# Optimization experiments

Hardware: AMD Instinct MI355X
Metric: run time of the kernel (lower is better)

Reference implementation:

```python
import jax, jax.numpy as jnp
import numpy as np

P, N, D = 8, 1024, 768
H = 12
HS = D // H
SCALE = float(HS ** 0.5)  # NOTE: original multiplies by sqrt(head_size)


def setup_inputs() -> dict:
    key = jax.random.key(0)
    k1, k2, k3 = jax.random.split(key, 3)
    pixel_values = jax.random.normal(k1, (P, N, D), dtype=jnp.float32)
    attention_mask = jnp.zeros((P, 1, 1, N), dtype=jnp.float32)
    qkv_w = jax.random.normal(k2, (D, 3 * D), dtype=jnp.float32) * 0.02
    qkv_b = jnp.zeros((3 * D,), dtype=jnp.float32)
    proj_w = jax.random.normal(k3, (D, D), dtype=jnp.float32) * 0.02
    proj_b = jnp.zeros((D,), dtype=jnp.float32)
    return {
        "pixel_values": pixel_values,
        "attention_mask": attention_mask,
        "qkv_w": qkv_w,
        "qkv_b": qkv_b,
        "proj_w": proj_w,
        "proj_b": proj_b,
    }


def reference(pixel_values, attention_mask, qkv_w, qkv_b, proj_w, proj_b):
    p, n, d = pixel_values.shape
    # fused QKV projection: (p, n, 3d) -> (3, p, H, n, hs)
    mixed = pixel_values @ qkv_w + qkv_b
    mixed = mixed.reshape(p, n, 3, H, HS).transpose(2, 0, 3, 1, 4)
    q, k, v = mixed[0], mixed[1], mixed[2]
    # scores: (p, H, n, n); original multiplies by sqrt(head_size)
    scores = jnp.einsum("phqd,phkd->phqk", q, k) * SCALE
    probs = jax.nn.softmax(scores, axis=-1)
    # dropout p=0 (identity in eval); mask added POST-softmax, per source
    probs = probs + attention_mask
    ctx = jnp.einsum("phqk,phkd->phqd", probs, v)
    ctx = ctx.transpose(0, 2, 1, 3).reshape(p, n, d)
    out = ctx @ proj_w + proj_b
    return out
```

## Files before the change

kernel.cpp:

```cpp
#include <hip/hip_runtime.h>
#include <hip/hip_bf16.h>
#include <cstdint>
#include <math.h>

constexpr int PB = 8;
constexpr int NS = 1024;
constexpr int DM = 768;
constexpr int NH = 12;
constexpr int HSZ = 64;
constexpr float EOFF = 88.0f;

typedef short bf16x8 __attribute__((ext_vector_type(8)));
typedef _Float16 half8 __attribute__((ext_vector_type(8)));
typedef float floatx4 __attribute__((ext_vector_type(4)));

__device__ __forceinline__ ushort f2bf(float x) {
    __hip_bfloat16 b = __float2bfloat16(x);
    return *reinterpret_cast<ushort*>(&b);
}
__device__ __forceinline__ float bf2f(ushort u) {
    __hip_bfloat16 b = *reinterpret_cast<__hip_bfloat16*>(&u);
    return __bfloat162float(b);
}
__device__ __forceinline__ ushort f2h(float x) {
    _Float16 h = (_Float16)x;
    return *reinterpret_cast<ushort*>(&h);
}

#define GLDS(g, l)                                                             \
    __builtin_amdgcn_global_load_lds(                                          \
        (const __attribute__((address_space(1))) void*)(g),                    \
        (__attribute__((address_space(3))) void*)(l), 16, 0, 0)

__global__ void split_kernel(const float* __restrict__ x, ushort* __restrict__ bh,
                             ushort* __restrict__ hf, int n4)
{
    int i = blockIdx.x * blockDim.x + threadIdx.x;
    const int stride = gridDim.x * blockDim.x;
    for (; i < n4; i += stride) {
        const float4 v = ((const float4*)x)[i];
        ((ushort4*)bh)[i] = ushort4{f2bf(v.x), f2bf(v.y), f2bf(v.z), f2bf(v.w)};
        ((ushort4*)hf)[i] = ushort4{f2h(v.x),  f2h(v.y),  f2h(v.z),  f2h(v.w)};
    }
}

__global__ void splitT_kernel(const float* __restrict__ w, ushort* __restrict__ bT,
                              ushort* __restrict__ fT, int K, int N)
{
    __shared__ float tile[32][33];
    const int tx = threadIdx.x, ty = threadIdx.y;
    const int bx = blockIdx.x, by = blockIdx.y;
    #pragma unroll
    for (int r = 0; r < 4; ++r)
        tile[ty + r*8][tx] = w[(size_t)(by*32 + ty + r*8) * N + bx*32 + tx];
    __syncthreads();
    #pragma unroll
    for (int r = 0; r < 4; ++r) {
        const int n = bx*32 + ty + r*8;
        const int k = by*32 + tx;
        const float v = tile[tx][ty + r*8];
        bT[(size_t)n * K + k] = f2bf(v);
        if (fT) fT[(size_t)n * K + k] = f2h(v);
    }
}

__global__ __launch_bounds__(256, 3)
void gemm_qkf(const ushort* __restrict__ Af, const ushort* __restrict__ Bf,
              const float* __restrict__ bias,
              ushort* __restrict__ qf, ushort* __restrict__ kf, int K)
{
    __shared__ __align__(16) ushort As[128*64];
    __shared__ __align__(16) ushort Bs[128*64];

    const int t    = threadIdx.x;
    const int w    = t >> 6;
    const int lane = t & 63;
    const int l15  = lane & 15;
    const int quad = lane >> 4;
    const int wm = w >> 1, wn = w & 1;
    const int m0 = blockIdx.x * 128, n0 = blockIdx.y * 128;

    floatx4 acc[4][4];
    #pragma unroll
    for (int i = 0; i < 4; ++i)
        #pragma unroll
        for (int j = 0; j < 4; ++j) acc[i][j] = floatx4{0.f, 0.f, 0.f, 0.f};

    const int srow8 = lane >> 3;
    const int sslot = lane & 7;

    for (int k0 = 0; k0 < K; k0 += 64) {
        #pragma unroll
        for (int j = 0; j < 4; ++j) {
            const int row = w*32 + j*8 + srow8;
            const int seg = sslot ^ (row & 7);
            const int ldst = (w*32 + j*8) * 64;
            GLDS(Af + (size_t)(m0 + row) * K + k0 + seg*8, As + ldst);
            GLDS(Bf + (size_t)(n0 + row) * K + k0 + seg*8, Bs + ldst);
        }
        __syncthreads();

        #pragma unroll
        for (int h2 = 0; h2 < 2; ++h2) {
            half8 fa[4], fb[4];
            #pragma unroll
            for (int i = 0; i < 4; ++i) {
                const int sl = ((h2*4 + quad) ^ (l15 & 7)) * 8;
                fa[i] = *(const half8*)(As + (wm*64 + i*16 + l15) * 64 + sl);
                fb[i] = *(const half8*)(Bs + (wn*64 + i*16 + l15) * 64 + sl);
            }
            #pragma unroll
            for (int mt = 0; mt < 4; ++mt)
                #pragma unroll
                for (int nt = 0; nt < 4; ++nt)
                    acc[mt][nt] = __builtin_amdgcn_mfma_f32_16x16x32_f16(fa[mt], fb[nt], acc[mt][nt], 0, 0, 0);
        }
        __syncthreads();
    }

    const int jbase = n0 + wn*64;
    const int c  = jbase / DM;
    const int hh = (jbase % DM) >> 6;
    const int pp = (m0 + wm*64) >> 10;
    const size_t head = (size_t)pp * NH + hh;
    ushort* dst = (c == 0 ? qf : kf);
    const float qscale = (c == 0) ? 8.0f : 1.0f;
    #pragma unroll
    for (int nt = 0; nt < 4; ++nt) {
        const int s = nt*16 + l15;
        const float bval = bias[jbase + s];
        #pragma unroll
        for (int mt = 0; mt < 4; ++mt) {
            const int tok0 = m0 + wm*64 + mt*16 + quad*4;
            const int nn0  = tok0 & 1023;
            #pragma unroll
            for (int r = 0; r < 4; ++r)
                dst[(head*NS + nn0 + r) * HSZ + s] = f2h((acc[mt][nt][r] + bval) * qscale);
        }
    }
}

template <int MODE>
__global__ __launch_bounds__(256, 3)
void gemm_1p(const ushort* __restrict__ Ah, const ushort* __restrict__ Bh,
             const float* __restrict__ bias, float* __restrict__ outf,
             ushort* __restrict__ vt, int K)
{
    __shared__ __align__(16) ushort As[128*64];
    __shared__ __align__(16) ushort Bs[128*64];

    const int t    = threadIdx.x;
    const int w    = t >> 6;
    const int lane = t & 63;
    const int l15  = lane & 15;
    const int quad = lane >> 4;
    const int wm = w >> 1, wn = w & 1;
    const int m0 = blockIdx.x * 128, n0 = blockIdx.y * 128;

    floatx4 acc[4][4];
    #pragma unroll
    for (int i = 0; i < 4; ++i)
        #pragma unroll
        for (int j = 0; j < 4; ++j) acc[i][j] = floatx4{0.f, 0.f, 0.f, 0.f};

    const int srow8 = lane >> 3;
    const int sslot = lane & 7;

    for (int k0 = 0; k0 < K; k0 += 64) {
        #pragma unroll
        for (int j = 0; j < 4; ++j) {
            const int row = w*32 + j*8 + srow8;
            const int seg = sslot ^ (row & 7);
            const int ldst = (w*32 + j*8) * 64;
            GLDS(Ah + (size_t)(m0 + row) * K + k0 + seg*8, As + ldst);
            GLDS(Bh + (size_t)(n0 + row) * K + k0 + seg*8, Bs + ldst);
        }
        __syncthreads();

        #pragma unroll
        for (int h2 = 0; h2 < 2; ++h2) {
            bf16x8 fa[4], fb[4];
            #pragma unroll
            for (int i = 0; i < 4; ++i) {
                const int sl = ((h2*4 + quad) ^ (l15 & 7)) * 8;
                fa[i] = *(const bf16x8*)(As + (wm*64 + i*16 + l15) * 64 + sl);
                fb[i] = *(const bf16x8*)(Bs + (wn*64 + i*16 + l15) * 64 + sl);
            }
            #pragma unroll
            for (int mt = 0; mt < 4; ++mt)
                #pragma unroll
                for (int nt = 0; nt < 4; ++nt)
                    acc[mt][nt] = __builtin_amdgcn_mfma_f32_16x16x32_bf16(fa[mt], fb[nt], acc[mt][nt], 0, 0, 0);
        }
        __syncthreads();
    }

    if (MODE == 0) {
        #pragma unroll
        for (int nt = 0; nt < 4; ++nt) {
            const int col = n0 + wn*64 + nt*16 + l15;
            const float bval = bias[col];
            #pragma unroll
            for (int mt = 0; mt < 4; ++mt) {
                const int row0 = m0 + wm*64 + mt*16 + quad*4;
                #pragma unroll
                for (int r = 0; r < 4; ++r)
                    outf[(size_t)(row0 + r) * DM + col] = acc[mt][nt][r] + bval;
            }
        }
    } else {
        const int jbase = n0 + wn*64;
        const int hh = jbase >> 6;
        const int pp = (m0 + wm*64) >> 10;
        const size_t head = (size_t)pp * NH + hh;
        #pragma unroll
        for (int nt = 0; nt < 4; ++nt) {
            const int s = nt*16 + l15;
            const float bval = bias[jbase + s];
            #pragma unroll
            for (int mt = 0; mt < 4; ++mt) {
                const int tok0 = m0 + wm*64 + mt*16 + quad*4;
                const int nn0  = tok0 & 1023;
                ushort4 pk;
                pk.x = f2bf(acc[mt][nt][0] + bval);
                pk.y = f2bf(acc[mt][nt][1] + bval);
                pk.z = f2bf(acc[mt][nt][2] + bval);
                pk.w = f2bf(acc[mt][nt][3] + bval);
                *(ushort4*)(vt + (head*HSZ + s) * NS + nn0) = pk;
            }
        }
    }
}

__global__ void mv_kernel(const float* __restrict__ mask, const ushort* __restrict__ vt,
                          float* __restrict__ mv)
{
    __shared__ float red[4][64];
    const int ph = blockIdx.x;
    const int t  = threadIdx.x;
    const int c  = t & 63, part = t >> 6;
    const ushort* vrow = vt + ((size_t)ph * HSZ + c) * NS + part * 256;
    const float*  mrow = mask + (size_t)(ph / NH) * NS + part * 256;
    float acc = 0.f;
    for (int k = 0; k < 256; k += 4) {
        const ushort4 v4 = *(const ushort4*)(vrow + k);
        const float4  m4 = *(const float4*)(mrow + k);
        acc += m4.x * bf2f(v4.x) + m4.y * bf2f(v4.y)
             + m4.z * bf2f(v4.z) + m4.w * bf2f(v4.w);
    }
    red[part][c] = acc;
    __syncthreads();
    if (t < 64)
        mv[(size_t)ph * HSZ + t] = red[0][t] + red[1][t] + red[2][t] + red[3][t];
}

__global__ __launch_bounds__(256, 5)
void attn_mfma_kernel(const ushort* __restrict__ qf, const ushort* __restrict__ kf,
                      const ushort* __restrict__ vt, const float* __restrict__ mv,
                      ushort* __restrict__ ctx)
{
    __shared__ __align__(16) ushort khs[64*64];
    __shared__ __align__(16) ushort vs [64*64];

    const int t    = threadIdx.x;
    const int w    = t >> 6;
    const int lane = t & 63;
    const int l15  = lane & 15;
    const int quad = lane >> 4;
    const int ph = blockIdx.x, qt = blockIdx.y;
    const int h  = ph % NH,    p  = ph / NH;
    const size_t headoff = ((size_t)p * NH + h) * (size_t)(NS * HSZ);

    const ushort* qb = qf + headoff + (size_t)(qt*64 + w*16 + l15) * HSZ + quad*8;
    const half8 qfr0 = *(const half8*)(qb);
    const half8 qfr1 = *(const half8*)(qb + 32);

    floatx4 o[4];
    float lsum = 0.f;
    #pragma unroll
    for (int tc = 0; tc < 4; ++tc) o[tc] = floatx4{0.f, 0.f, 0.f, 0.f};

    const int srow8 = lane >> 3;
    const int sslot = lane & 7;
    const int xs = l15 & 7;

    for (int kt = 0; kt < 16; ++kt) {
        __syncthreads();
        #pragma unroll
        for (int j = 0; j < 2; ++j) {
            const int row  = w*16 + j*8 + srow8;
            const int segK = sslot ^ ((row & 3) | (((row >> 3) & 1) << 2));
            const int segV = sslot ^ (row & 7);
            const size_t gk = headoff + (size_t)(kt*64 + row) * HSZ + segK*8;
            const size_t gv = headoff + (size_t)row * NS + kt*64 + segV*8;
            const int ldst = (w*16 + j*8) * 64;
            GLDS(kf + gk, khs + ldst);
            GLDS(vt + gv, vs  + ldst);
        }
        __syncthreads();

        bf16x8 bp[2];
        #pragma unroll
        for (int tt = 0; tt < 4; ++tt) {
            const int rho = ((l15 >> 2) << 3) + ((tt & 1) << 2) + (l15 & 3) + ((tt >> 1) << 5);
            const int a0 = rho*64 + ((quad       ^ xs) * 8);
            const int a1 = rho*64 + (((quad | 4) ^ xs) * 8);
            const half8 bh0 = *(const half8*)(khs + a0);
            const half8 bh1 = *(const half8*)(khs + a1);
            floatx4 a = floatx4{0.f, 0.f, 0.f, 0.f};
            a = __builtin_amdgcn_mfma_f32_16x16x32_f16(bh0, qfr0, a, 0, 0, 0);
            a = __builtin_amdgcn_mfma_f32_16x16x32_f16(bh1, qfr1, a, 0, 0, 0);
            const float e0 = __expf(a[0] - EOFF);
            const float e1 = __expf(a[1] - EOFF);
            const float e2 = __expf(a[2] - EOFF);
            const float e3 = __expf(a[3] - EOFF);
            lsum += (e0 + e1) + (e2 + e3);
            bf16x8& dst = bp[tt >> 1];
            const int off = (tt & 1) * 4;
            dst[off + 0] = (short)f2bf(e0);
            dst[off + 1] = (short)f2bf(e1);
            dst[off + 2] = (short)f2bf(e2);
            dst[off + 3] = (short)f2bf(e3);
        }

        #pragma unroll
        for (int tc = 0; tc < 4; ++tc) {
            const int crow = (tc*16 + l15) * 64;
            const bf16x8 va0 = *(const bf16x8*)(vs + crow + ((quad       ^ xs) * 8));
            const bf16x8 va1 = *(const bf16x8*)(vs + crow + (((quad | 4) ^ xs) * 8));
            o[tc] = __builtin_amdgcn_mfma_f32_16x16x32_bf16(va0, bp[0], o[tc], 0, 0, 0);
            o[tc] = __builtin_amdgcn_mfma_f32_16x16x32_bf16(va1, bp[1], o[tc], 0, 0, 0);
        }
    }

    float l = lsum;
    l += __shfl_xor(l, 16);
    l += __shfl_xor(l, 32);
    const float inv = 1.0f / l;

    const float* mvp = mv + ((size_t)p * NH + h) * HSZ;
    const int row = qt*64 + w*16 + l15;
    const size_t base = ((size_t)p * NS + row) * DM + h * 64;
    #pragma unroll
    for (int tc = 0; tc < 4; ++tc) {
        const int c0 = tc*16 + quad*4;
        ushort4 pk;
        pk.x = f2bf(o[tc][0] * inv + mvp[c0 + 0]);
        pk.y = f2bf(o[tc][1] * inv + mvp[c0 + 1]);
        pk.z = f2bf(o[tc][2] * inv + mvp[c0 + 2]);
        pk.w = f2bf(o[tc][3] * inv + mvp[c0 + 3]);
        *(ushort4*)(ctx + base + c0) = pk;
    }
}

extern "C" void kernel_launch(void* const* d_in, const int* in_sizes, int n_in,
                              void* d_out, int out_size, void* d_ws, size_t ws_size,
                              hipStream_t stream)
{
    const float* x      = (const float*)d_in[0];
    const float* mask   = (const float*)d_in[1];
    const float* qkv_w  = (const float*)d_in[2];
    const float* qkv_b  = (const float*)d_in[3];
    const float* proj_w = (const float*)d_in[4];
    const float* proj_b = (const float*)d_in[5];
    float* out = (float*)d_out;

    const size_t HE = (size_t)PB * NH * NS * HSZ;
    const size_t QW = (size_t)DM * 3 * DM;
    const size_t PW = (size_t)DM * DM;
    ushort* xh  = (ushort*)d_ws;
    ushort* xf  = xh + HE;
    ushort* qwh = xf + HE;
    ushort* qwf = qwh + QW;
    ushort* pwh = qwf + QW;
    ushort* qfv = pwh + PW;
    ushort* kfv = qfv + HE;
    ushort* vtv = kfv + HE;
    float*  mvb = (float*)(vtv + HE);
    ushort* cth = xh;

    split_kernel<<<2048, 256, 0, stream>>>(x, xh, xf, (int)(HE / 4));
    splitT_kernel<<<dim3(3*DM/32, DM/32), dim3(32, 8), 0, stream>>>(qkv_w, qwh, qwf, DM, 3*DM);
    splitT_kernel<<<dim3(DM/32,   DM/32), dim3(32, 8), 0, stream>>>(proj_w, pwh, nullptr, DM, DM);

    gemm_qkf<<<dim3(PB*NS/128, 12), 256, 0, stream>>>(
        xf, qwf, qkv_b, qfv, kfv, DM);
    gemm_1p<2><<<dim3(PB*NS/128, DM/128), 256, 0, stream>>>(
        xh, qwh + (size_t)2*DM*DM, qkv_b + 2*DM, nullptr, vtv, DM);

    mv_kernel<<<dim3(PB*NH), 256, 0, stream>>>(mask, vtv, mvb);

    attn_mfma_kernel<<<dim3(PB*NH, NS/64), 256, 0, stream>>>(
        qfv, kfv, vtv, mvb, cth);

    gemm_1p<0><<<dim3(PB*NS/128, DM/128), 256, 0, stream>>>(
        cth, pwh, proj_b, out, nullptr, DM);
}
```

Before: 207.6 us.

## Fuse QKV projections into one fp16 GEMM and drop bf16 input copies

Merges the separate Q/K fp16 GEMM and V bf16 GEMM into one templated fp16 GEMM launch covering all 3*D columns. The bf16 copies of x and the weights are no longer produced, which removes a conversion pass and its memory traffic. Softmax switches to exp2 with log2(e) folded into the Q scale and the offset preloaded into the MFMA accumulator. Context is now written as packed fp16 and the output projection runs in fp16 as well. The change trades bf16 range for fp16 precision on x, V and context.

```diff
diff --git a/kernel.cpp b/kernel.cpp
--- a/kernel.cpp
+++ b/kernel.cpp
@@ -8,12 +8,28 @@
 constexpr int DM = 768;
 constexpr int NH = 12;
 constexpr int HSZ = 64;
-constexpr float EOFF = 88.0f;
-
-typedef short bf16x8 __attribute__((ext_vector_type(8)));
-typedef _Float16 half8 __attribute__((ext_vector_type(8)));
-typedef float floatx4 __attribute__((ext_vector_type(4)));
-
+constexpr float QS    = 11.541560327111707f;
+constexpr float EOFFL = 126.95716359822878f;
+
+typedef short    bf16x8 __attribute__((ext_vector_type(8)));
+typedef _Float16 half8  __attribute__((ext_vector_type(8)));
+typedef __fp16   fp16x2 __attribute__((ext_vector_type(2)));
+typedef float    floatx4 __attribute__((ext_vector_type(4)));
+
+#if __has_builtin(__builtin_amdgcn_exp2f)
+#define EXP2(x) __builtin_amdgcn_exp2f(x)
+#else
+#define EXP2(x) exp2f(x)
+#endif
+
+__device__ __forceinline__ ushort f2h(float x) {
+    _Float16 h = (_Float16)x;
+    return *reinterpret_cast<ushort*>(&h);
+}
+__device__ __forceinline__ float h2f(ushort u) {
+    _Float16 h = __builtin_bit_cast(_Float16, u);
+    return (float)h;
+}
 __device__ __forceinline__ ushort f2bf(float x) {
     __hip_bfloat16 b = __float2bfloat16(x);
     return *reinterpret_cast<ushort*>(&b);
@@ -22,9 +38,9 @@
     __hip_bfloat16 b = *reinterpret_cast<__hip_bfloat16*>(&u);
     return __bfloat162float(b);
 }
-__device__ __forceinline__ ushort f2h(float x) {
-    _Float16 h = (_Float16)x;
-    return *reinterpret_cast<ushort*>(&h);
+__device__ __forceinline__ unsigned int pk2h(float a, float b) {
+    fp16x2 h = __builtin_amdgcn_cvt_pkrtz(a, b);
+    return __builtin_bit_cast(unsigned int, h);
 }
 
 #define GLDS(g, l)                                                             \
@@ -32,20 +48,19 @@
         (const __attribute__((address_space(1))) void*)(g),                    \
         (__attribute__((address_space(3))) void*)(l), 16, 0, 0)
 
-__global__ void split_kernel(const float* __restrict__ x, ushort* __restrict__ bh,
-                             ushort* __restrict__ hf, int n4)
+__global__ void split_kernel(const float* __restrict__ x, ushort* __restrict__ hf,
+                             int n4)
 {
     int i = blockIdx.x * blockDim.x + threadIdx.x;
     const int stride = gridDim.x * blockDim.x;
     for (; i < n4; i += stride) {
         const float4 v = ((const float4*)x)[i];
-        ((ushort4*)bh)[i] = ushort4{f2bf(v.x), f2bf(v.y), f2bf(v.z), f2bf(v.w)};
-        ((ushort4*)hf)[i] = ushort4{f2h(v.x),  f2h(v.y),  f2h(v.z),  f2h(v.w)};
-    }
-}
-
-__global__ void splitT_kernel(const float* __restrict__ w, ushort* __restrict__ bT,
-                              ushort* __restrict__ fT, int K, int N)
+        ((ushort4*)hf)[i] = ushort4{f2h(v.x), f2h(v.y), f2h(v.z), f2h(v.w)};
+    }
+}
+
+__global__ void splitT_kernel(const float* __restrict__ w, ushort* __restrict__ fT,
+                              int K, int N)
 {
     __shared__ float tile[32][33];
     const int tx = threadIdx.x, ty = threadIdx.y;
@@ -58,16 +73,16 @@
     for (int r = 0; r < 4; ++r) {
         const int n = bx*32 + ty + r*8;
         const int k = by*32 + tx;
-        const float v = tile[tx][ty + r*8];
-        bT[(size_t)n * K + k] = f2bf(v);
-        if (fT) fT[(size_t)n * K + k] = f2h(v);
-    }
-}
-
+        fT[(size_t)n * K + k] = f2h(tile[tx][ty + r*8]);
+    }
+}
+
+template <int MODE>
 __global__ __launch_bounds__(256, 3)
-void gemm_qkf(const ushort* __restrict__ Af, const ushort* __restrict__ Bf,
-              const float* __restrict__ bias,
-              ushort* __restrict__ qf, ushort* __restrict__ kf, int K)
+void gemm_f16(const ushort* __restrict__ Af, const ushort* __restrict__ Bf,
+              const float* __restrict__ bias, float* __restrict__ outf,
+              ushort* __restrict__ qf, ushort* __restrict__ kf,
+              ushort* __restrict__ vt, int K)
 {
     __shared__ __align__(16) ushort As[128*64];
     __shared__ __align__(16) ushort Bs[128*64];
@@ -118,83 +133,6 @@
         __syncthreads();
     }
 
-    const int jbase = n0 + wn*64;
-    const int c  = jbase / DM;
-    const int hh = (jbase % DM) >> 6;
-    const int pp = (m0 + wm*64) >> 10;
-    const size_t head = (size_t)pp * NH + hh;
-    ushort* dst = (c == 0 ? qf : kf);
-    const float qscale = (c == 0) ? 8.0f : 1.0f;
-    #pragma unroll
-    for (int nt = 0; nt < 4; ++nt) {
-        const int s = nt*16 + l15;
-        const float bval = bias[jbase + s];
-        #pragma unroll
-        for (int mt = 0; mt < 4; ++mt) {
-            const int tok0 = m0 + wm*64 + mt*16 + quad*4;
-            const int nn0  = tok0 & 1023;
-            #pragma unroll
-            for (int r = 0; r < 4; ++r)
-                dst[(head*NS + nn0 + r) * HSZ + s] = f2h((acc[mt][nt][r] + bval) * qscale);
-        }
-    }
-}
-
-template <int MODE>
-__global__ __launch_bounds__(256, 3)
-void gemm_1p(const ushort* __restrict__ Ah, const ushort* __restrict__ Bh,
-             const float* __restrict__ bias, float* __restrict__ outf,
-             ushort* __restrict__ vt, int K)
-{
-    __shared__ __align__(16) ushort As[128*64];
-    __shared__ __align__(16) ushort Bs[128*64];
-
-    const int t    = threadIdx.x;
-    const int w    = t >> 6;
-    const int lane = t & 63;
-    const int l15  = lane & 15;
-    const int quad = lane >> 4;
-    const int wm = w >> 1, wn = w & 1;
-    const int m0 = blockIdx.x * 128, n0 = blockIdx.y * 128;
-
-    floatx4 acc[4][4];
-    #pragma unroll
-    for (int i = 0; i < 4; ++i)
-        #pragma unroll
-        for (int j = 0; j < 4; ++j) acc[i][j] = floatx4{0.f, 0.f, 0.f, 0.f};
-
-    const int srow8 = lane >> 3;
-    const int sslot = lane & 7;
-
-    for (int k0 = 0; k0 < K; k0 += 64) {
-        #pragma unroll
-        for (int j = 0; j < 4; ++j) {
-            const int row = w*32 + j*8 + srow8;
-            const int seg = sslot ^ (row & 7);
-            const int ldst = (w*32 + j*8) * 64;
-            GLDS(Ah + (size_t)(m0 + row) * K + k0 + seg*8, As + ldst);
-            GLDS(Bh + (size_t)(n0 + row) * K + k0 + seg*8, Bs + ldst);
-        }
-        __syncthreads();
-
-        #pragma unroll
-        for (int h2 = 0; h2 < 2; ++h2) {
-            bf16x8 fa[4], fb[4];
-            #pragma unroll
-            for (int i = 0; i < 4; ++i) {
-                const int sl = ((h2*4 + quad) ^ (l15 & 7)) * 8;
-                fa[i] = *(const bf16x8*)(As + (wm*64 + i*16 + l15) * 64 + sl);
-                fb[i] = *(const bf16x8*)(Bs + (wn*64 + i*16 + l15) * 64 + sl);
-            }
-            #pragma unroll
-            for (int mt = 0; mt < 4; ++mt)
-                #pragma unroll
-                for (int nt = 0; nt < 4; ++nt)
-                    acc[mt][nt] = __builtin_amdgcn_mfma_f32_16x16x32_bf16(fa[mt], fb[nt], acc[mt][nt], 0, 0, 0);
-        }
-        __syncthreads();
-    }
-
     if (MODE == 0) {
         #pragma unroll
         for (int nt = 0; nt < 4; ++nt) {
@@ -210,23 +148,42 @@
         }
     } else {
         const int jbase = n0 + wn*64;
-        const int hh = jbase >> 6;
+        const int c  = jbase / DM;
+        const int hh = (jbase % DM) >> 6;
         const int pp = (m0 + wm*64) >> 10;
         const size_t head = (size_t)pp * NH + hh;
-        #pragma unroll
-        for (int nt = 0; nt < 4; ++nt) {
-            const int s = nt*16 + l15;
-            const float bval = bias[jbase + s];
-            #pragma unroll
-            for (int mt = 0; mt < 4; ++mt) {
-                const int tok0 = m0 + wm*64 + mt*16 + quad*4;
-                const int nn0  = tok0 & 1023;
-                ushort4 pk;
-                pk.x = f2bf(acc[mt][nt][0] + bval);
-                pk.y = f2bf(acc[mt][nt][1] + bval);
-                pk.z = f2bf(acc[mt][nt][2] + bval);
-                pk.w = f2bf(acc[mt][nt][3] + bval);
-                *(ushort4*)(vt + (head*HSZ + s) * NS + nn0) = pk;
+        if (c < 2) {
+            ushort* dst = (c == 0 ? qf : kf);
+            const float qscale = (c == 0) ? QS : 1.0f;
+            #pragma unroll
+            for (int nt = 0; nt < 4; ++nt) {
+                const int s = nt*16 + l15;
+                const float bval = bias[jbase + s];
+                #pragma unroll
+                for (int mt = 0; mt < 4; ++mt) {
+                    const int tok0 = m0 + wm*64 + mt*16 + quad*4;
+                    const int nn0  = tok0 & 1023;
+                    #pragma unroll
+                    for (int r = 0; r < 4; ++r)
+                        dst[(head*NS + nn0 + r) * HSZ + s] = f2h((acc[mt][nt][r] + bval) * qscale);
+                }
+            }
+        } else {
+            #pragma unroll
+            for (int nt = 0; nt < 4; ++nt) {
+                const int s = nt*16 + l15;
+                const float bval = bias[jbase + s];
+                #pragma unroll
+                for (int mt = 0; mt < 4; ++mt) {
+                    const int tok0 = m0 + wm*64 + mt*16 + quad*4;
+                    const int nn0  = tok0 & 1023;
+                    ushort4 pk;
+                    pk.x = f2bf(acc[mt][nt][0] + bval);
+                    pk.y = f2bf(acc[mt][nt][1] + bval);
+                    pk.z = f2bf(acc[mt][nt][2] + bval);
+                    pk.w = f2bf(acc[mt][nt][3] + bval);
+                    *(ushort4*)(vt + (head*HSZ + s) * NS + nn0) = pk;
+                }
             }
         }
     }
@@ -307,13 +264,13 @@
             const int a1 = rho*64 + (((quad | 4) ^ xs) * 8);
             const half8 bh0 = *(const half8*)(khs + a0);
             const half8 bh1 = *(const half8*)(khs + a1);
-            floatx4 a = floatx4{0.f, 0.f, 0.f, 0.f};
+            floatx4 a = floatx4{-EOFFL, -EOFFL, -EOFFL, -EOFFL};
             a = __builtin_amdgcn_mfma_f32_16x16x32_f16(bh0, qfr0, a, 0, 0, 0);
             a = __builtin_amdgcn_mfma_f32_16x16x32_f16(bh1, qfr1, a, 0, 0, 0);
-            const float e0 = __expf(a[0] - EOFF);
-            const float e1 = __expf(a[1] - EOFF);
-            const float e2 = __expf(a[2] - EOFF);
-            const float e3 = __expf(a[3] - EOFF);
+            const float e0 = EXP2(a[0]);
+            const float e1 = EXP2(a[1]);
+            const float e2 = EXP2(a[2]);
+            const float e3 = EXP2(a[3]);
             lsum += (e0 + e1) + (e2 + e3);
             bf16x8& dst = bp[tt >> 1];
             const int off = (tt & 1) * 4;
@@ -344,12 +301,12 @@
     #pragma unroll
     for (int tc = 0; tc < 4; ++tc) {
         const int c0 = tc*16 + quad*4;
-        ushort4 pk;
-        pk.x = f2bf(o[tc][0] * inv + mvp[c0 + 0]);
-        pk.y = f2bf(o[tc][1] * inv + mvp[c0 + 1]);
-        pk.z = f2bf(o[tc][2] * inv + mvp[c0 + 2]);
-        pk.w = f2bf(o[tc][3] * inv + mvp[c0 + 3]);
-        *(ushort4*)(ctx + base + c0) = pk;
+        const unsigned int lo = pk2h(o[tc][0] * inv + mvp[c0 + 0],
+                                     o[tc][1] * inv + mvp[c0 + 1]);
+        const unsigned int hi = pk2h(o[tc][2] * inv + mvp[c0 + 2],
+                                     o[tc][3] * inv + mvp[c0 + 3]);
+        uint2 st; st.x = lo; st.y = hi;
+        *(uint2*)(ctx + base + c0) = st;
     }
 }
 
@@ -368,31 +325,27 @@
     const size_t HE = (size_t)PB * NH * NS * HSZ;
     const size_t QW = (size_t)DM * 3 * DM;
     const size_t PW = (size_t)DM * DM;
-    ushort* xh  = (ushort*)d_ws;
-    ushort* xf  = xh + HE;
-    ushort* qwh = xf + HE;
-    ushort* qwf = qwh + QW;
-    ushort* pwh = qwf + QW;
-    ushort* qfv = pwh + PW;
+    ushort* xf  = (ushort*)d_ws;
+    ushort* qwf = xf + HE;
+    ushort* pwf = qwf + QW;
+    ushort* qfv = pwf + PW;
     ushort* kfv = qfv + HE;
     ushort* vtv = kfv + HE;
     float*  mvb = (float*)(vtv + HE);
-    ushort* cth = xh;
-
-    split_kernel<<<2048, 256, 0, stream>>>(x, xh, xf, (int)(HE / 4));
-    splitT_kernel<<<dim3(3*DM/32, DM/32), dim3(32, 8), 0, stream>>>(qkv_w, qwh, qwf, DM, 3*DM);
-    splitT_kernel<<<dim3(DM/32,   DM/32), dim3(32, 8), 0, stream>>>(proj_w, pwh, nullptr, DM, DM);
-
-    gemm_qkf<<<dim3(PB*NS/128, 12), 256, 0, stream>>>(
-        xf, qwf, qkv_b, qfv, kfv, DM);
-    gemm_1p<2><<<dim3(PB*NS/128, DM/128), 256, 0, stream>>>(
-        xh, qwh + (size_t)2*DM*DM, qkv_b + 2*DM, nullptr, vtv, DM);
+    ushort* cth = xf;
+
+    split_kernel<<<2048, 256, 0, stream>>>(x, xf, (int)(HE / 4));
+    splitT_kernel<<<dim3(3*DM/32, DM/32), dim3(32, 8), 0, stream>>>(qkv_w, qwf, DM, 3*DM);
+    splitT_kernel<<<dim3(DM/32,   DM/32), dim3(32, 8), 0, stream>>>(proj_w, pwf, DM, DM);
+
+    gemm_f16<1><<<dim3(PB*NS/128, 3*DM/128), 256, 0, stream>>>(
+        xf, qwf, qkv_b, nullptr, qfv, kfv, vtv, DM);
 
     mv_kernel<<<dim3(PB*NH), 256, 0, stream>>>(mask, vtv, mvb);
 
     attn_mfma_kernel<<<dim3(PB*NH, NS/64), 256, 0, stream>>>(
         qfv, kfv, vtv, mvb, cth);
 
-    gemm_1p<0><<<dim3(PB*NS/128, DM/128), 256, 0, stream>>>(
-        cth, pwh, proj_b, out, nullptr, DM);
-}
+    gemm_f16<0><<<dim3(PB*NS/128, DM/128), 256, 0, stream>>>(
+        cth, pwf, proj_b, out, nullptr, nullptr, nullptr, DM);
+}
```

Result: faster. 201.0 us (-3.2%).
